# Kernel tuning notes

Measured on AMD Instinct MI355X. Metric: run time of the kernel, lower is better.

Reference implementation:

```python
import jax, jax.numpy as jnp
import numpy as np


def setup_inputs() -> dict:
    key = jax.random.key(0)
    k1, k2, k3, k4 = jax.random.split(key, 4)
    B, S, IN, H = 4, 2048, 512, 1024
    x = jax.random.normal(k1, (B, S, IN), dtype=jnp.float32)
    W1 = jax.random.normal(k2, (IN, H), dtype=jnp.float32) * (1.0 / np.sqrt(IN))
    b1 = jax.random.normal(k3, (H,), dtype=jnp.float32) * 0.02
    Wq = jax.random.normal(k4, (H, H), dtype=jnp.float32) * (1.0 / np.sqrt(H))
    return {"x": x, "W1": W1, "b1": b1, "Wq": Wq, "atten_size": 16}


def reference(x, W1, b1, Wq, atten_size):
    A = atten_size
    B, S, _ = x.shape
    H = W1.shape[1]
    h = jax.nn.relu(jnp.einsum('bsi,ih->bsh', x, W1) + b1)  # [B,S,H]
    # zero-pad sequence dim by A on each side
    padded = jnp.pad(h, ((0, 0), (A, A), (0, 0)))  # [B,S+2A,H]
    # torch: stack(roll(padded, k, 1) for k in -A..A, dim=2) then slice [A:-A]
    # => x_nei[b, i, j] = padded[b, 2A + i - j]
    idx = 2 * A + jnp.arange(S)[:, None] - jnp.arange(2 * A + 1)[None, :]  # [S,W]
    x_nei = padded[:, idx, :]  # [B,S,W,H]
    q = jnp.einsum('bsh,hk->bsk', h, Wq)  # [B,S,H]
    scores = jnp.einsum('bsh,bswh->bsw', q, x_nei) / jnp.sqrt(jnp.asarray(H, x.dtype))
    w = jax.nn.softmax(scores, axis=2)  # softmax over window axis
    out = jnp.einsum('bsw,bswh->bsh', w, x_nei)
    return out
```

## Files before the change

### kernel.cpp

```cpp
#include <hip/hip_runtime.h>
#include <stdint.h>

constexpr int BATCH = 4;
constexpr int SEQ   = 2048;
constexpr int DIN   = 512;
constexpr int DH    = 1024;
constexpr int BS    = BATCH * SEQ;
constexpr int AP    = 32;
constexpr int AW    = 64;

typedef float  floatx4 __attribute__((ext_vector_type(4)));
typedef short  bf16x8  __attribute__((ext_vector_type(8)));

static __device__ __forceinline__ unsigned short f2bf(float f) {
  union { float f; unsigned u; } v; v.f = f;
  unsigned r = (v.u + 0x7fffu + ((v.u >> 16) & 1u)) >> 16;
  return (unsigned short)r;
}

static __device__ __forceinline__ void gld_lds16(const unsigned short* g, const short* l) {
  typedef const __attribute__((address_space(1))) void* gvp;
  typedef __attribute__((address_space(3))) void* lvp;
  __builtin_amdgcn_global_load_lds((gvp)(uintptr_t)g, (lvp)(unsigned)(uintptr_t)l, 16, 0, 0);
}

__global__ __launch_bounds__(256) void to_bf16_k(const float* __restrict__ in,
                                                 unsigned short* __restrict__ out, int n) {
  int i = (blockIdx.x * 256 + threadIdx.x) * 4;
  if (i < n) {
    float4 v = *(const float4*)(in + i);
    ushort4 o;
    o.x = f2bf(v.x); o.y = f2bf(v.y); o.z = f2bf(v.z); o.w = f2bf(v.w);
    *(ushort4*)(out + i) = o;
  }
}

__global__ __launch_bounds__(256) void transpose_bf16_k(const float* __restrict__ in,
                                                        unsigned short* __restrict__ out,
                                                        int R, int C) {
  __shared__ float t[32][33];
  int c0 = blockIdx.x * 32, r0 = blockIdx.y * 32;
  int tx = threadIdx.x & 31, ty = threadIdx.x >> 5;
  for (int i = ty; i < 32; i += 8) t[i][tx] = in[(size_t)(r0 + i) * C + c0 + tx];
  __syncthreads();
  for (int i = ty; i < 32; i += 8) out[(size_t)(c0 + i) * R + r0 + tx] = f2bf(t[tx][i]);
}

__global__ __launch_bounds__(256) void transpose_hb_k(const unsigned short* __restrict__ in,
                                                      unsigned short* __restrict__ out) {
  __shared__ __align__(16) unsigned short t[64][80];
  const int tid = threadIdx.x;
  const int r0 = blockIdx.x * 64;
  const int c0 = blockIdx.y * 64;
  const int tr = tid >> 2, tc = (tid & 3) * 16;
  const uint4* src = (const uint4*)(in + (size_t)(r0 + tr) * DH + c0 + tc);
  uint4 v0 = src[0], v1 = src[1];
  *(uint4*)&t[tr][tc]     = v0;
  *(uint4*)&t[tr][tc + 8] = v1;
  __syncthreads();
  __align__(16) unsigned short vals[16];
  #pragma unroll
  for (int e = 0; e < 16; e++) vals[e] = t[tc + e][tr];
  uint4* dst = (uint4*)(out + (size_t)(c0 + tr) * BS + r0 + tc);
  dst[0] = ((uint4*)vals)[0];
  dst[1] = ((uint4*)vals)[1];
}

template <bool RELU>
__global__ __launch_bounds__(256) void gemm_bt(const unsigned short* __restrict__ Ab,
                                               const unsigned short* __restrict__ Bt,
                                               const float* __restrict__ bias,
                                               unsigned short* __restrict__ outB,
                                               int M, int N, int K) {
  __shared__ __align__(16) short As[128 * 32];
  __shared__ __align__(16) short Bs[128 * 32];
  const int tid  = threadIdx.x;
  const int m0   = blockIdx.y * 128, n0 = blockIdx.x * 128;
  const int wv   = tid >> 6, lane = tid & 63;
  const int wm   = (wv >> 1) * 64, wn = (wv & 1) * 64;
  const int l16  = lane & 15, quad = lane >> 4;

  const int ra = lane >> 2;
  const int ca = (lane & 3) * 8;
  const unsigned short* gA0 = Ab + (size_t)(m0 + wv * 32 + ra) * K + ca;
  const unsigned short* gA1 = Ab + (size_t)(m0 + wv * 32 + 16 + ra) * K + ca;
  const unsigned short* gB0 = Bt + (size_t)(n0 + wv * 32 + ra) * K + ca;
  const unsigned short* gB1 = Bt + (size_t)(n0 + wv * 32 + 16 + ra) * K + ca;
  const short* lA0 = &As[wv * 1024];
  const short* lA1 = &As[wv * 1024 + 512];
  const short* lB0 = &Bs[wv * 1024];
  const short* lB1 = &Bs[wv * 1024 + 512];

  floatx4 acc[4][4];
  for (int i = 0; i < 4; i++)
    for (int j = 0; j < 4; j++) acc[i][j] = {0.f, 0.f, 0.f, 0.f};

  const int ksteps = K >> 5;
  for (int ks = 0; ks < ksteps; ++ks) {
    __syncthreads();
    gld_lds16(gA0, lA0); gld_lds16(gA1, lA1);
    gld_lds16(gB0, lB0); gld_lds16(gB1, lB1);
    gA0 += 32; gA1 += 32; gB0 += 32; gB1 += 32;
    __syncthreads();
    bf16x8 af[4], bfr[4];
    for (int i = 0; i < 4; i++)
      af[i] = *(const bf16x8*)&As[(wm + i * 16 + l16) * 32 + quad * 8];
    for (int j = 0; j < 4; j++)
      bfr[j] = *(const bf16x8*)&Bs[(wn + j * 16 + l16) * 32 + quad * 8];
    for (int i = 0; i < 4; i++)
      for (int j = 0; j < 4; j++)
        acc[i][j] = __builtin_amdgcn_mfma_f32_16x16x32_bf16(af[i], bfr[j], acc[i][j], 0, 0, 0);
  }

  for (int j = 0; j < 4; j++) {
    const int col = n0 + wn + j * 16 + l16;
    const float bv = RELU ? bias[col] : 0.f;
    for (int i = 0; i < 4; i++) {
      const int rowb = m0 + wm + i * 16 + quad * 4;
      for (int r = 0; r < 4; r++) {
        float v = acc[i][j][r] + bv;
        if (RELU) v = fmaxf(v, 0.f);
        outB[(size_t)(rowb + r) * N + col] = f2bf(v);
      }
    }
  }
}

__global__ __launch_bounds__(512) void attn_mfma_k(const unsigned short* __restrict__ hb,
                                                   const unsigned short* __restrict__ hbT,
                                                   const unsigned short* __restrict__ qb,
                                                   float* __restrict__ out) {
  __shared__ __align__(16) short Qs[32 * 72];
  __shared__ __align__(16) short Hs[64 * 72];
  __shared__ __align__(16) short Ps[32 * 72];
  __shared__ __align__(16) short Ht[128 * 72];
  __shared__ float Sf[32 * 64];

  const int tid  = threadIdx.x;
  const int wave = tid >> 6, lane = tid & 63;
  const int l16  = lane & 15, quad = lane >> 4;
  const int p0   = blockIdx.x * AP;
  const int s0   = p0 & (SEQ - 1);

  for (int i = tid; i < 32 * 72 / 2; i += 512) ((unsigned*)Ps)[i] = 0;

  const int mtile = wave >> 2;
  const int ntile = wave & 3;
  const bool isQ = tid < 128;
  const bool isH = (tid >= 128) && (tid < 384);
  const int sq = tid & 3;
  int srow = isQ ? (tid >> 2) : ((tid - 128) >> 2);
  bool ldv = false;
  const uint4* gsrc = nullptr;
  short* ldst = nullptr;
  if (isQ) {
    ldv = true;
    gsrc = (const uint4*)(qb + (size_t)(p0 + srow) * DH + sq * 16);
    ldst = &Qs[srow * 72 + sq * 16];
  } else if (isH) {
    const int hj = s0 - 16 + srow;
    ldv = (hj >= 0) && (hj < SEQ);
    gsrc = (const uint4*)(hb + (long long)(p0 - 16 + srow) * DH + sq * 16);
    ldst = &Hs[srow * 72 + sq * 16];
  }

  floatx4 acc = {0.f, 0.f, 0.f, 0.f};
  for (int ks = 0; ks < DH / 64; ++ks) {
    uint4 r0 = {0, 0, 0, 0}, r1 = {0, 0, 0, 0};
    if (ldv) { r0 = gsrc[0]; r1 = gsrc[1]; gsrc += 8; }
    __syncthreads();
    if (isQ || isH) { ((uint4*)ldst)[0] = r0; ((uint4*)ldst)[1] = r1; }
    __syncthreads();
    bf16x8 a0 = *(const bf16x8*)&Qs[(mtile * 16 + l16) * 72 + quad * 8];
    bf16x8 a1 = *(const bf16x8*)&Qs[(mtile * 16 + l16) * 72 + 32 + quad * 8];
    bf16x8 b0 = *(const bf16x8*)&Hs[(ntile * 16 + l16) * 72 + quad * 8];
    bf16x8 b1 = *(const bf16x8*)&Hs[(ntile * 16 + l16) * 72 + 32 + quad * 8];
    acc = __builtin_amdgcn_mfma_f32_16x16x32_bf16(a0, b0, acc, 0, 0, 0);
    acc = __builtin_amdgcn_mfma_f32_16x16x32_bf16(a1, b1, acc, 0, 0, 0);
  }
  for (int r = 0; r < 4; r++)
    Sf[(mtile * 16 + quad * 4 + r) * 64 + ntile * 16 + l16] = acc[r] * (1.f / 32.f);
  __syncthreads();

  {
    const int row = tid >> 4, k = tid & 15;
    const float v0 = Sf[row * 64 + row + k];
    const float v1 = Sf[row * 64 + row + k + 16];
    const float v2 = (k == 0) ? Sf[row * 64 + row + 32] : -1e30f;
    float mx = fmaxf(v0, fmaxf(v1, v2));
    for (int off = 1; off < 16; off <<= 1) mx = fmaxf(mx, __shfl_xor(mx, off, 64));
    const float e0 = __expf(v0 - mx), e1 = __expf(v1 - mx);
    const float e2 = (k == 0) ? __expf(v2 - mx) : 0.f;
    float sum = e0 + e1 + e2;
    for (int off = 1; off < 16; off <<= 1) sum += __shfl_xor(sum, off, 64);
    const float inv = 1.f / sum;
    Ps[row * 72 + row + k] = f2bf(e0 * inv);
    Ps[row * 72 + row + k + 16] = f2bf(e1 * inv);
    if (k == 0) Ps[row * 72 + row + 32] = f2bf(e2 * inv);
  }
  __syncthreads();

  const bf16x8 pa0 = *(const bf16x8*)&Ps[(mtile * 16 + l16) * 72 + quad * 8];
  const bf16x8 pa1 = *(const bf16x8*)&Ps[(mtile * 16 + l16) * 72 + 32 + quad * 8];

  int lo = 16 - s0; if (lo < 0) lo = 0;
  int hi = SEQ + 16 - s0; if (hi > AW) hi = AW;
  const bool interior = (lo == 0) && (hi == AW);
  const int hn = tid >> 2;
  const int ntp = (wave & 3) * 2;

  for (int c = 0; c < DH / 128; ++c) {
    const int nc = c * 128;
    const unsigned short* hp = hbT + ((long long)(nc + hn) * BS + p0 - 16 + sq * 16);
    uint4 r0 = ((const uint4*)hp)[0], r1 = ((const uint4*)hp)[1];
    if (!interior) {
      unsigned short vals[16];
      ((uint4*)vals)[0] = r0; ((uint4*)vals)[1] = r1;
      #pragma unroll
      for (int e = 0; e < 16; e++) {
        const int k = sq * 16 + e;
        if (k < lo || k >= hi) vals[e] = 0;
      }
      r0 = ((uint4*)vals)[0]; r1 = ((uint4*)vals)[1];
    }
    __syncthreads();
    ((uint4*)&Ht[hn * 72 + sq * 16])[0] = r0;
    ((uint4*)&Ht[hn * 72 + sq * 16])[1] = r1;
    __syncthreads();
    floatx4 acc2[2] = {{0.f, 0.f, 0.f, 0.f}, {0.f, 0.f, 0.f, 0.f}};
    for (int t = 0; t < 2; t++) {
      const int nt = ntp + t;
      bf16x8 b0 = *(const bf16x8*)&Ht[(nt * 16 + l16) * 72 + quad * 8];
      bf16x8 b1 = *(const bf16x8*)&Ht[(nt * 16 + l16) * 72 + 32 + quad * 8];
      acc2[t] = __builtin_amdgcn_mfma_f32_16x16x32_bf16(pa0, b0, acc2[t], 0, 0, 0);
      acc2[t] = __builtin_amdgcn_mfma_f32_16x16x32_bf16(pa1, b1, acc2[t], 0, 0, 0);
    }
    for (int t = 0; t < 2; t++) {
      const int col = nc + (ntp + t) * 16 + l16;
      for (int r = 0; r < 4; r++)
        out[(size_t)(p0 + mtile * 16 + quad * 4 + r) * DH + col] = acc2[t][r];
    }
  }
}

extern "C" void kernel_launch(void* const* d_in, const int* in_sizes, int n_in,
                              void* d_out, int out_size, void* d_ws, size_t ws_size,
                              hipStream_t stream) {
  const float* x  = (const float*)d_in[0];
  const float* W1 = (const float*)d_in[1];
  const float* b1 = (const float*)d_in[2];
  const float* Wq = (const float*)d_in[3];

  char* w = (char*)d_ws;
  unsigned short* xb  = (unsigned short*)(w);
  unsigned short* w1t = (unsigned short*)(w + (8ull  << 20));
  unsigned short* wqt = (unsigned short*)(w + (9ull  << 20));
  unsigned short* hb  = (unsigned short*)(w + (11ull << 20));
  unsigned short* hbT = (unsigned short*)(w + (27ull << 20));
  unsigned short* qb  = (unsigned short*)(w + (43ull << 20));

  to_bf16_k<<<(BS * DIN) / (256 * 4), 256, 0, stream>>>(x, xb, BS * DIN);
  transpose_bf16_k<<<dim3(DH / 32, DIN / 32), 256, 0, stream>>>(W1, w1t, DIN, DH);
  transpose_bf16_k<<<dim3(DH / 32, DH / 32), 256, 0, stream>>>(Wq, wqt, DH, DH);

  gemm_bt<true><<<dim3(DH / 128, BS / 128), 256, 0, stream>>>(xb, w1t, b1, hb, BS, DH, DIN);
  transpose_hb_k<<<dim3(BS / 64, DH / 64), 256, 0, stream>>>(hb, hbT);
  gemm_bt<false><<<dim3(DH / 128, BS / 128), 256, 0, stream>>>(hb, wqt, nullptr, qb, BS, DH, DH);

  attn_mfma_k<<<BS / AP, 512, 0, stream>>>(hb, hbT, qb, (float*)d_out);
}
```

Before: 172.4 us.

## Load MFMA operands directly from global memory in attention kernel, drop LDS staging

The score phase now has each wave read Q and H fragments straight from global memory into MFMA registers. It spreads the K loop over four independent accumulators and removes the per-step LDS stores and two barriers per iteration. The output phase swaps operand roles so the transposed H is the A operand and P is the B operand, which lets each lane write a contiguous float4 of the output. It also drops the Ht LDS staging and its barriers. This cuts LDS traffic and synchronisation but relies on uncoalesced 16-byte global loads and L2 reuse across waves.

Result: no change. 174.3 us (+1.1%).

```diff
diff --git a/kernel.cpp b/kernel.cpp
--- a/kernel.cpp
+++ b/kernel.cpp
@@ -130,11 +130,8 @@
                                                    const unsigned short* __restrict__ hbT,
                                                    const unsigned short* __restrict__ qb,
                                                    float* __restrict__ out) {
-  __shared__ __align__(16) short Qs[32 * 72];
-  __shared__ __align__(16) short Hs[64 * 72];
+  __shared__ float Sf[32 * 64];
   __shared__ __align__(16) short Ps[32 * 72];
-  __shared__ __align__(16) short Ht[128 * 72];
-  __shared__ float Sf[32 * 64];
 
   const int tid  = threadIdx.x;
   const int wave = tid >> 6, lane = tid & 63;
@@ -144,42 +141,28 @@
 
   for (int i = tid; i < 32 * 72 / 2; i += 512) ((unsigned*)Ps)[i] = 0;
 
-  const int mtile = wave >> 2;
-  const int ntile = wave & 3;
-  const bool isQ = tid < 128;
-  const bool isH = (tid >= 128) && (tid < 384);
-  const int sq = tid & 3;
-  int srow = isQ ? (tid >> 2) : ((tid - 128) >> 2);
-  bool ldv = false;
-  const uint4* gsrc = nullptr;
-  short* ldst = nullptr;
-  if (isQ) {
-    ldv = true;
-    gsrc = (const uint4*)(qb + (size_t)(p0 + srow) * DH + sq * 16);
-    ldst = &Qs[srow * 72 + sq * 16];
-  } else if (isH) {
-    const int hj = s0 - 16 + srow;
-    ldv = (hj >= 0) && (hj < SEQ);
-    gsrc = (const uint4*)(hb + (long long)(p0 - 16 + srow) * DH + sq * 16);
-    ldst = &Hs[srow * 72 + sq * 16];
-  }
-
-  floatx4 acc = {0.f, 0.f, 0.f, 0.f};
-  for (int ks = 0; ks < DH / 64; ++ks) {
-    uint4 r0 = {0, 0, 0, 0}, r1 = {0, 0, 0, 0};
-    if (ldv) { r0 = gsrc[0]; r1 = gsrc[1]; gsrc += 8; }
-    __syncthreads();
-    if (isQ || isH) { ((uint4*)ldst)[0] = r0; ((uint4*)ldst)[1] = r1; }
-    __syncthreads();
-    bf16x8 a0 = *(const bf16x8*)&Qs[(mtile * 16 + l16) * 72 + quad * 8];
-    bf16x8 a1 = *(const bf16x8*)&Qs[(mtile * 16 + l16) * 72 + 32 + quad * 8];
-    bf16x8 b0 = *(const bf16x8*)&Hs[(ntile * 16 + l16) * 72 + quad * 8];
-    bf16x8 b1 = *(const bf16x8*)&Hs[(ntile * 16 + l16) * 72 + 32 + quad * 8];
-    acc = __builtin_amdgcn_mfma_f32_16x16x32_bf16(a0, b0, acc, 0, 0, 0);
-    acc = __builtin_amdgcn_mfma_f32_16x16x32_bf16(a1, b1, acc, 0, 0, 0);
-  }
-  for (int r = 0; r < 4; r++)
-    Sf[(mtile * 16 + quad * 4 + r) * 64 + ntile * 16 + l16] = acc[r] * (1.f / 32.f);
+  {
+    const int mt = wave >> 2, nt = wave & 3;
+    const unsigned short* qp = qb + (size_t)(p0 + mt * 16 + l16) * DH + quad * 8;
+    const int hrow = s0 - 16 + nt * 16 + l16;
+    const bool hv = (hrow >= 0) && (hrow < SEQ);
+    const unsigned short* hp = hb + (long long)(p0 - 16 + nt * 16 + l16) * DH + quad * 8;
+
+    floatx4 ac[4] = {{0,0,0,0},{0,0,0,0},{0,0,0,0},{0,0,0,0}};
+    const bf16x8 hz = {0,0,0,0,0,0,0,0};
+    #pragma unroll
+    for (int it = 0; it < 32; ++it) {
+      bf16x8 qa = *(const bf16x8*)(qp + it * 32);
+      bf16x8 ha = hz;
+      if (hv) ha = *(const bf16x8*)(hp + it * 32);
+      ac[it & 3] = __builtin_amdgcn_mfma_f32_16x16x32_bf16(qa, ha, ac[it & 3], 0, 0, 0);
+    }
+    floatx4 s4;
+    for (int r = 0; r < 4; r++)
+      s4[r] = (ac[0][r] + ac[1][r]) + (ac[2][r] + ac[3][r]);
+    for (int r = 0; r < 4; r++)
+      Sf[(mt * 16 + quad * 4 + r) * 64 + nt * 16 + l16] = s4[r] * (1.f / 32.f);
+  }
   __syncthreads();
 
   {
@@ -200,45 +183,34 @@
   }
   __syncthreads();
 
-  const bf16x8 pa0 = *(const bf16x8*)&Ps[(mtile * 16 + l16) * 72 + quad * 8];
-  const bf16x8 pa1 = *(const bf16x8*)&Ps[(mtile * 16 + l16) * 72 + 32 + quad * 8];
-
-  int lo = 16 - s0; if (lo < 0) lo = 0;
-  int hi = SEQ + 16 - s0; if (hi > AW) hi = AW;
-  const bool interior = (lo == 0) && (hi == AW);
-  const int hn = tid >> 2;
-  const int ntp = (wave & 3) * 2;
-
-  for (int c = 0; c < DH / 128; ++c) {
-    const int nc = c * 128;
-    const unsigned short* hp = hbT + ((long long)(nc + hn) * BS + p0 - 16 + sq * 16);
-    uint4 r0 = ((const uint4*)hp)[0], r1 = ((const uint4*)hp)[1];
-    if (!interior) {
-      unsigned short vals[16];
-      ((uint4*)vals)[0] = r0; ((uint4*)vals)[1] = r1;
-      #pragma unroll
-      for (int e = 0; e < 16; e++) {
-        const int k = sq * 16 + e;
-        if (k < lo || k >= hi) vals[e] = 0;
+  {
+    const int nt2 = wave >> 2;
+    const bf16x8 pb0 = *(const bf16x8*)&Ps[(nt2 * 16 + l16) * 72 + quad * 8];
+    const bf16x8 pb1 = *(const bf16x8*)&Ps[(nt2 * 16 + l16) * 72 + 32 + quad * 8];
+
+    int lo = 16 - s0; if (lo < 0) lo = 0;
+    int hi = SEQ + 16 - s0; if (hi > AW) hi = AW;
+    const bool interior = (lo == 0) && (hi == AW);
+
+    #pragma unroll
+    for (int i = 0; i < 16; ++i) {
+      const int mt2 = (wave & 3) * 16 + i;
+      const unsigned short* ap = hbT + (size_t)(mt2 * 16 + l16) * BS + (p0 - 16) + quad * 8;
+      bf16x8 aa0 = *(const bf16x8*)(ap);
+      bf16x8 aa1 = *(const bf16x8*)(ap + 32);
+      if (!interior) {
+        #pragma unroll
+        for (int j = 0; j < 8; j++) {
+          const int k = quad * 8 + j;
+          if (k < lo || k >= hi) aa0[j] = 0;
+          if (k + 32 < lo || k + 32 >= hi) aa1[j] = 0;
+        }
       }
-      r0 = ((uint4*)vals)[0]; r1 = ((uint4*)vals)[1];
-    }
-    __syncthreads();
-    ((uint4*)&Ht[hn * 72 + sq * 16])[0] = r0;
-    ((uint4*)&Ht[hn * 72 + sq * 16])[1] = r1;
-    __syncthreads();
-    floatx4 acc2[2] = {{0.f, 0.f, 0.f, 0.f}, {0.f, 0.f, 0.f, 0.f}};
-    for (int t = 0; t < 2; t++) {
-      const int nt = ntp + t;
-      bf16x8 b0 = *(const bf16x8*)&Ht[(nt * 16 + l16) * 72 + quad * 8];
-      bf16x8 b1 = *(const bf16x8*)&Ht[(nt * 16 + l16) * 72 + 32 + quad * 8];
-      acc2[t] = __builtin_amdgcn_mfma_f32_16x16x32_bf16(pa0, b0, acc2[t], 0, 0, 0);
-      acc2[t] = __builtin_amdgcn_mfma_f32_16x16x32_bf16(pa1, b1, acc2[t], 0, 0, 0);
-    }
-    for (int t = 0; t < 2; t++) {
-      const int col = nc + (ntp + t) * 16 + l16;
-      for (int r = 0; r < 4; r++)
-        out[(size_t)(p0 + mtile * 16 + quad * 4 + r) * DH + col] = acc2[t][r];
+      floatx4 o = {0.f, 0.f, 0.f, 0.f};
+      o = __builtin_amdgcn_mfma_f32_16x16x32_bf16(aa0, pb0, o, 0, 0, 0);
+      o = __builtin_amdgcn_mfma_f32_16x16x32_bf16(aa1, pb1, o, 0, 0, 0);
+      float4 st; st.x = o[0]; st.y = o[1]; st.z = o[2]; st.w = o[3];
+      *(float4*)(out + (size_t)(p0 + nt2 * 16 + l16) * DH + mt2 * 16 + quad * 4) = st;
     }
   }
 }
```
